# Kernel optimization log

Hardware: AMD Instinct MI355X
Metric: run time of the kernel (lower is better)

## Reference

```python
import jax, jax.numpy as jnp
import numpy as np

EMBED_DIM = 384
HEADS = 6
HEAD_DIM = EMBED_DIM // HEADS
WINDOW = 64


def setup_inputs() -> dict:
    key = jax.random.key(0)
    ks = jax.random.split(key, 5)
    B, T = 128, 256
    s_attn = 1.0 / np.sqrt(EMBED_DIM)
    x = jax.random.normal(ks[0], (B, T, EMBED_DIM), dtype=jnp.float32)
    W_attn = jax.random.normal(ks[1], (EMBED_DIM, 3 * EMBED_DIM), dtype=jnp.float32) * s_attn
    b_attn = jax.random.normal(ks[2], (3 * EMBED_DIM,), dtype=jnp.float32) * 0.02
    W_proj = jax.random.normal(ks[3], (EMBED_DIM, EMBED_DIM), dtype=jnp.float32) * s_attn
    b_proj = jax.random.normal(ks[4], (EMBED_DIM,), dtype=jnp.float32) * 0.02
    return {"x": x, "W_attn": W_attn, "b_attn": b_attn, "W_proj": W_proj, "b_proj": b_proj}


def reference(x, W_attn, b_attn, W_proj, b_proj):
    B, T, C = x.shape
    qkv = x @ W_attn + b_attn  # [B,T,3C]
    q, k, v = jnp.split(qkv, 3, axis=-1)
    # [B, H, T, hd]
    q = q.reshape(B, T, HEADS, HEAD_DIM).transpose(0, 2, 1, 3)
    k = k.reshape(B, T, HEADS, HEAD_DIM).transpose(0, 2, 1, 3)
    v = v.reshape(B, T, HEADS, HEAD_DIM).transpose(0, 2, 1, 3)
    scale = 1.0 / np.sqrt(HEAD_DIM).astype(np.float32)
    att = jnp.einsum('bhqd,bhkd->bhqk', q, k) * scale
    i = jnp.arange(T)
    causal = i[:, None] >= i[None, :]
    local = jnp.abs(i[:, None] - i[None, :]) <= WINDOW
    mask = (causal & local)[None, None, :, :]
    att = jnp.where(mask, att, -jnp.inf)
    att = jax.nn.softmax(att, axis=-1)
    y = jnp.einsum('bhqk,bhkd->bhqd', att, v)
    y = y.transpose(0, 2, 1, 3).reshape(B, T, C)
    return y @ W_proj + b_proj
```

## Files before the change

kernel.cpp:

```cpp
#include <hip/hip_runtime.h>

#define B_SZ   128
#define T_SEQ  256
#define C_DIM  384
#define HEADS  6
#define HD     64
#define WIN    64

typedef __bf16 bf16x8 __attribute__((ext_vector_type(8)));
typedef float  f32x4  __attribute__((ext_vector_type(4)));

typedef __attribute__((address_space(3))) void lds_void;
typedef __attribute__((address_space(1))) void gbl_void;

__device__ __forceinline__ unsigned short f2bf(float f) {
  unsigned u = __float_as_uint(f);
  u += 0x7FFFu + ((u >> 16) & 1u);
  return (unsigned short)(u >> 16);
}


__global__ __launch_bounds__(256) void convert_pack_f32_bf16(
    const float* __restrict__ in, unsigned short* __restrict__ out) {
  const int tid = blockIdx.x * 256 + threadIdx.x;
  const int m   = tid / 48;
  const int rem = tid % 48;
  const int kc  = rem >> 2;
  const int u   = rem & 3;
  const float4 a = *(const float4*)(in + (size_t)m * 384 + kc * 32 + u * 8);
  const float4 b = *(const float4*)(in + (size_t)m * 384 + kc * 32 + u * 8 + 4);
  const int p = u ^ ((m & 7) >> 1);
  unsigned short* dst =
      out + ((size_t)(m >> 7) * 12 + kc) * 4096 + (m & 127) * 32 + p * 8;
  ushort4 o1, o2;
  o1.x = f2bf(a.x); o1.y = f2bf(a.y); o1.z = f2bf(a.z); o1.w = f2bf(a.w);
  o2.x = f2bf(b.x); o2.y = f2bf(b.y); o2.z = f2bf(b.z); o2.w = f2bf(b.w);
  *(ushort4*)dst = o1;
  *(ushort4*)(dst + 4) = o2;
}

__global__ __launch_bounds__(256) void transpose_convert_pack(
    const float* __restrict__ in, unsigned short* __restrict__ out,
    int K, int N) {
  __shared__ float tile[32][33];
  const int gx = blockIdx.x * 32;
  const int gy = blockIdx.y * 32;
  const int tx = threadIdx.x;
  const int ty = threadIdx.y;
#pragma unroll
  for (int r = ty; r < 32; r += 8)
    tile[r][tx] = in[(size_t)(gy + r) * N + gx + tx];
  __syncthreads();
  const int nkc = K >> 5;
#pragma unroll
  for (int r = ty; r < 32; r += 8) {
    const int n = gx + r;
    const int k = gy + tx;
    const int p = (((k >> 3) & 3) ^ ((n & 7) >> 1));
    out[((size_t)(n >> 7) * nkc + (k >> 5)) * 4096 + (n & 127) * 32 + p * 8 +
        (k & 7)] = f2bf(tile[tx][r]);
  }
}

template <bool OUT_BF16, int KK>
__global__ __launch_bounds__(512, 4) void gemm_mfma_bf16(
    const unsigned short* __restrict__ A,
    const unsigned short* __restrict__ Bt,
    const float* __restrict__ bias,
    void* __restrict__ Cv, int M, int N, int tiles_n) {
  __shared__ __attribute__((aligned(16))) char smem_raw[73728];
  float* ep = (float*)smem_raw;

  constexpr int NK = KK / 32;

  const int t    = threadIdx.x;
  const int lane = t & 63;
  const int w    = t >> 6;
  const int wr   = w >> 1;
  const int wc   = w & 1;

  const unsigned id    = blockIdx.x;
  const unsigned remap = (id & 7u) * (gridDim.x >> 3) + (id >> 3);
  const int by = remap / (unsigned)tiles_n;
  const int bx = remap % (unsigned)tiles_n;
  const int m0 = by * 256;
  const int n0 = bx * 128;

  const unsigned short* Ap0 = A  + (size_t)(by * 2)     * NK * 4096;
  const unsigned short* Ap1 = A  + (size_t)(by * 2 + 1) * NK * 4096;
  const unsigned short* Btile = Bt + (size_t)bx * NK * 4096;

  const int m16  = lane & 15;
  const int quad = lane >> 4;
  const int cp   = (quad ^ ((m16 >> 1) & 3)) << 3;

  f32x4 acc[4][4];
#pragma unroll
  for (int i = 0; i < 4; ++i)
#pragma unroll
    for (int j = 0; j < 4; ++j) acc[i][j] = (f32x4){0.f, 0.f, 0.f, 0.f};

  auto stage = [&](int slot, int kc) {
    unsigned short* As = (unsigned short*)(smem_raw + slot * 24576);
    unsigned short* Bs = As + 256 * 32;
#pragma unroll
    for (int i = 0; i < 3; ++i) {
      const int idx = w * 3 + i;
      if (idx < 16) {
        const unsigned short* src =
            ((idx >> 3) ? Ap1 : Ap0) + (size_t)kc * 4096 + (idx & 7) * 512 +
            lane * 8;
        __builtin_amdgcn_global_load_lds((const gbl_void*)src,
                                         (lds_void*)(As + idx * 512), 16, 0, 0);
      } else {
        const int sub = idx - 16;
        const unsigned short* src =
            Btile + (size_t)kc * 4096 + sub * 512 + lane * 8;
        __builtin_amdgcn_global_load_lds((const gbl_void*)src,
                                         (lds_void*)(Bs + sub * 512), 16, 0, 0);
      }
    }
  };

  stage(0, 0);
  stage(1, 1);

#pragma unroll
  for (int kt = 0; kt < NK; ++kt) {
    if (kt + 1 < NK)
      asm volatile("s_waitcnt vmcnt(3) lgkmcnt(0)" ::: "memory");
    else
      asm volatile("s_waitcnt vmcnt(0) lgkmcnt(0)" ::: "memory");
    __builtin_amdgcn_s_barrier();
    __builtin_amdgcn_sched_barrier(0);

    if (kt + 2 < NK) stage((kt + 2) % 3, kt + 2);

    const unsigned short* As =
        (const unsigned short*)(smem_raw + (kt % 3) * 24576);
    const unsigned short* Bs = As + 256 * 32;

    bf16x8 af[4];
#pragma unroll
    for (int mt = 0; mt < 4; ++mt)
      af[mt] = *(const bf16x8*)(As + (size_t)(wr * 64 + mt * 16 + m16) * 32 + cp);
#pragma unroll
    for (int nt = 0; nt < 4; ++nt) {
      bf16x8 bfr = *(const bf16x8*)(Bs + (size_t)(wc * 64 + nt * 16 + m16) * 32 + cp);
#pragma unroll
      for (int mt = 0; mt < 4; ++mt)
        acc[mt][nt] = __builtin_amdgcn_mfma_f32_16x16x32_bf16(
            af[mt], bfr, acc[mt][nt], 0, 0, 0);
    }
  }
  __syncthreads();

  float bv[4];
#pragma unroll
  for (int nt = 0; nt < 4; ++nt) bv[nt] = bias[n0 + wc * 64 + nt * 16 + m16];

  const int which = bx / 3;
  const int hbase = (bx % 3) * 2;

#pragma unroll
  for (int p = 0; p < 4; ++p) {
    if (p) __syncthreads();
    if (wr == p) {
#pragma unroll
      for (int mt = 0; mt < 4; ++mt)
#pragma unroll
        for (int nt = 0; nt < 4; ++nt)
#pragma unroll
          for (int r = 0; r < 4; ++r)
            ep[(mt * 16 + quad * 4 + r) * 132 + wc * 64 + nt * 16 + m16] =
                acc[mt][nt][r] + bv[nt];
    }
    __syncthreads();
#pragma unroll
    for (int cc = 0; cc < 4; ++cc) {
      const int chunk = cc * 512 + t;
      const int row = chunk >> 5;
      const int c4  = chunk & 31;
      const int grow = m0 + p * 64 + row;
      if (OUT_BF16) {
        const int hh  = c4 >> 4;
        const int g16 = c4 & 15;
        const int s   = (which == 2) ? 0 : (row & 7);
        const int col = hh * 64 + ((((g16 >> 1) ^ s) << 3) | ((g16 & 1) << 2));
        f32x4 v = *(const f32x4*)(ep + row * 132 + col);
        ushort4 o;
        o.x = f2bf(v[0]); o.y = f2bf(v[1]); o.z = f2bf(v[2]); o.w = f2bf(v[3]);
        const int b_ = grow >> 8;
        const int tp = grow & 255;
        *(ushort4*)((unsigned short*)Cv +
                    ((size_t)((b_ * 3 + which) * HEADS + hbase + hh) * T_SEQ +
                     tp) * HD + g16 * 4) = o;
      } else {
        f32x4 v = *(const f32x4*)(ep + row * 132 + c4 * 4);
        const int gcol = n0 + c4 * 4;
        *(f32x4*)((float*)Cv + (size_t)grow * N + gcol) = v;
      }
    }
  }
}

#define PSTR 68
__global__ __launch_bounds__(256) void attn_mfma(
    const unsigned short* __restrict__ qkv, unsigned short* __restrict__ y) {
  __shared__ unsigned short Qs[64 * 64];
  __shared__ unsigned short Ks[64 * 64];
  __shared__ unsigned short Vt[64 * 64];
  __shared__ float Pw[4][16 * PSTR];

  const unsigned id  = blockIdx.x;
  const unsigned bid = (id & 7u) * (gridDim.x >> 3) + (id >> 3);
  const int qt  = bid & 3;
  const int h   = (bid >> 2) % HEADS;
  const int b   = bid / (4 * HEADS);
  const int t   = threadIdx.x;
  const int lane = t & 63;
  const int w    = t >> 6;
  const int quad = lane >> 4;
  const int m16  = lane & 15;
  const int sw   = m16 & 7;

  const unsigned short* Qpane =
      qkv + ((size_t)((b * 3 + 0) * HEADS + h) * T_SEQ) * HD;
  const unsigned short* Kpane =
      qkv + ((size_t)((b * 3 + 1) * HEADS + h) * T_SEQ) * HD;
  const unsigned short* Vpane =
      qkv + ((size_t)((b * 3 + 2) * HEADS + h) * T_SEQ) * HD;
  const int qg0 = qt * 64;

#pragma unroll
  for (int i = 0; i < 2; ++i) {
    const int inst = w * 2 + i;
    __builtin_amdgcn_global_load_lds(
        (const gbl_void*)(Qpane + (size_t)qg0 * HD + inst * 512 + lane * 8),
        (lds_void*)(Qs + inst * 512), 16, 0, 0);
  }

  float m_r[4], l_r[4];
  f32x4 yacc[4];
#pragma unroll
  for (int r = 0; r < 4; ++r) { m_r[r] = -1e30f; l_r[r] = 0.f; }
#pragma unroll
  for (int dt = 0; dt < 4; ++dt) yacc[dt] = (f32x4){0.f, 0.f, 0.f, 0.f};

  const int nchunks  = (qt == 0) ? 1 : 2;
  const int kb_first = (qt == 0) ? 0 : (qg0 - 64);
  const int qrow_base = qg0 + w * 16 + quad * 4;

  for (int ch = 0; ch < nchunks; ++ch) {
    const int kb = kb_first + ch * 64;

    __syncthreads();

#pragma unroll
    for (int i = 0; i < 2; ++i) {
      const int inst = w * 2 + i;
      __builtin_amdgcn_global_load_lds(
          (const gbl_void*)(Kpane + (size_t)kb * HD + inst * 512 + lane * 8),
          (lds_void*)(Ks + inst * 512), 16, 0, 0);
    }
    {
      const int vkey = t & 63;
      const int kc = vkey >> 3, ke = vkey & 7;
      const int vd0  = (t >> 6) * 16;
      const unsigned short* gv = Vpane + (size_t)(kb + vkey) * HD + vd0;
#pragma unroll
      for (int u = 0; u < 4; ++u) {
        ushort4 vv = *(const ushort4*)(gv + u * 4);
#pragma unroll
        for (int jj = 0; jj < 4; ++jj) {
          const int d = vd0 + u * 4 + jj;
          const unsigned short val =
              (jj == 0) ? vv.x : (jj == 1) ? vv.y : (jj == 2) ? vv.z : vv.w;
          Vt[d * 64 + ((kc ^ (d & 7)) << 3) + ke] = val;
        }
      }
    }
    __syncthreads();

    f32x4 sacc[4];
#pragma unroll
    for (int nt = 0; nt < 4; ++nt) sacc[nt] = (f32x4){0.f, 0.f, 0.f, 0.f};
#pragma unroll
    for (int ks = 0; ks < 64; ks += 32) {
      const int cp = (((ks >> 3) + quad) ^ sw) << 3;
      bf16x8 aq = *(const bf16x8*)(Qs + (size_t)(w * 16 + m16) * 64 + cp);
#pragma unroll
      for (int nt = 0; nt < 4; ++nt) {
        bf16x8 kf = *(const bf16x8*)(Ks + (size_t)(nt * 16 + m16) * 64 + cp);
        sacc[nt] = __builtin_amdgcn_mfma_f32_16x16x32_bf16(aq, kf, sacc[nt], 0, 0, 0);
      }
    }

    float mc[4] = {-1e30f, -1e30f, -1e30f, -1e30f};
#pragma unroll
    for (int nt = 0; nt < 4; ++nt) {
      const int kg = kb + nt * 16 + m16;
#pragma unroll
      for (int r = 0; r < 4; ++r) {
        const int qg = qrow_base + r;
        const bool valid = (kg <= qg) && (qg - kg <= WIN);
        const float sv = valid ? (sacc[nt][r] * 0.125f) : -1e30f;
        sacc[nt][r] = sv;
        mc[r] = fmaxf(mc[r], sv);
      }
    }
#pragma unroll
    for (int r = 0; r < 4; ++r) {
#pragma unroll
      for (int x = 1; x <= 8; x <<= 1) mc[r] = fmaxf(mc[r], __shfl_xor(mc[r], x));
    }

#pragma unroll
    for (int r = 0; r < 4; ++r) {
      const float mn    = fmaxf(m_r[r], mc[r]);
      const float alpha = __expf(m_r[r] - mn);
      m_r[r] = mn;
      l_r[r] *= alpha;
#pragma unroll
      for (int dt = 0; dt < 4; ++dt) yacc[dt][r] *= alpha;
      float ls = 0.f;
#pragma unroll
      for (int nt = 0; nt < 4; ++nt) {
        const float p = __expf(sacc[nt][r] - mn);
        sacc[nt][r] = p;
        ls += p;
      }
#pragma unroll
      for (int x = 1; x <= 8; x <<= 1) ls += __shfl_xor(ls, x);
      l_r[r] += ls;
    }

#pragma unroll
    for (int nt = 0; nt < 4; ++nt)
#pragma unroll
      for (int r = 0; r < 4; ++r)
        Pw[w][(quad * 4 + r) * PSTR + nt * 16 + m16] = sacc[nt][r];

#pragma unroll
    for (int ks = 0; ks < 64; ks += 32) {
      f32x4 pa = *(const f32x4*)(&Pw[w][m16 * PSTR + ks + quad * 8]);
      f32x4 pb = *(const f32x4*)(&Pw[w][m16 * PSTR + ks + quad * 8 + 4]);
      bf16x8 ap;
#pragma unroll
      for (int j = 0; j < 4; ++j) {
        ap[j]     = (__bf16)pa[j];
        ap[4 + j] = (__bf16)pb[j];
      }
      const int cp = (((ks >> 3) + quad) ^ sw) << 3;
#pragma unroll
      for (int dt = 0; dt < 4; ++dt) {
        bf16x8 vf = *(const bf16x8*)(Vt + (size_t)(dt * 16 + m16) * 64 + cp);
        yacc[dt] = __builtin_amdgcn_mfma_f32_16x16x32_bf16(ap, vf, yacc[dt], 0, 0, 0);
      }
    }
  }

  float* epy = &Pw[0][0];
  float inv[4];
#pragma unroll
  for (int r = 0; r < 4; ++r) inv[r] = 1.f / l_r[r];
#pragma unroll
  for (int dt = 0; dt < 4; ++dt)
#pragma unroll
    for (int r = 0; r < 4; ++r)
      epy[(w * 16 + quad * 4 + r) * PSTR + dt * 16 + m16] = yacc[dt][r] * inv[r];
  __syncthreads();
#pragma unroll
  for (int cc = 0; cc < 4; ++cc) {
    const int chunk = cc * 256 + t;
    const int row = chunk >> 4;
    const int c4  = chunk & 15;
    f32x4 v = *(const f32x4*)(epy + row * PSTR + c4 * 4);
    ushort4 o;
    o.x = f2bf(v[0]); o.y = f2bf(v[1]); o.z = f2bf(v[2]); o.w = f2bf(v[3]);
    const int m = b * T_SEQ + qg0 + row;
    const int c = h * HD + c4 * 4;
    const int kc = c >> 5;
    const int u  = (c >> 3) & 3;
    const int p  = u ^ ((m & 7) >> 1);
    *(ushort4*)(y + ((size_t)(m >> 7) * 12 + kc) * 4096 + (m & 127) * 32 +
                p * 8 + (c & 7)) = o;
  }
}

extern "C" void kernel_launch(void* const* d_in, const int* in_sizes, int n_in,
                              void* d_out, int out_size, void* d_ws, size_t ws_size,
                              hipStream_t stream) {
  const float* x      = (const float*)d_in[0];
  const float* W_attn = (const float*)d_in[1];
  const float* b_attn = (const float*)d_in[2];
  const float* W_proj = (const float*)d_in[3];
  const float* b_proj = (const float*)d_in[4];
  float* out = (float*)d_out;

  const int M = B_SZ * T_SEQ;

  unsigned short* qkv_b = (unsigned short*)d_ws;
  unsigned short* y_b   = qkv_b + (size_t)M * (3 * C_DIM);
  unsigned short* x_b   = y_b   + (size_t)M * C_DIM;
  unsigned short* Wa_t  = x_b   + (size_t)M * C_DIM;
  unsigned short* Wp_t  = Wa_t  + (size_t)(3 * C_DIM) * C_DIM;

  {
    convert_pack_f32_bf16<<<dim3(M * 48 / 256), 256, 0, stream>>>(x, x_b);
    transpose_convert_pack<<<dim3((3 * C_DIM) / 32, C_DIM / 32), dim3(32, 8), 0,
                             stream>>>(W_attn, Wa_t, C_DIM, 3 * C_DIM);
    transpose_convert_pack<<<dim3(C_DIM / 32, C_DIM / 32), dim3(32, 8), 0,
                             stream>>>(W_proj, Wp_t, C_DIM, C_DIM);
  }

  gemm_mfma_bf16<true, C_DIM><<<dim3(9 * (M / 256)), 512, 0, stream>>>(
      x_b, Wa_t, b_attn, qkv_b, M, 3 * C_DIM, 9);

  attn_mfma<<<dim3(B_SZ * HEADS * (T_SEQ / 64)), 256, 0, stream>>>(qkv_b, y_b);

  gemm_mfma_bf16<false, C_DIM><<<dim3(3 * (M / 256)), 512, 0, stream>>>(
      y_b, Wp_t, b_proj, out, M, C_DIM, 3);
}
```

Before: 189.3 us.

## Fuse fp32-to-bf16 conversion of x into the QKV GEMM A-tile loader

Removes the separate x conversion kernel and its bf16 staging buffer. The QKV GEMM now reads fp32 x straight into registers, converts it to bf16 and writes swizzled LDS tiles, while B still arrives through global_load_lds with a triple-buffered pipeline and manual waitcnt/barrier scheduling. This saves one launch plus a full write and re-read of x in bf16. In exchange the GEMM reads twice as many A bytes (fp32), each of the 9 column tiles converts the same rows again, and it needs more registers.

```diff
diff --git a/kernel.cpp b/kernel.cpp
--- a/kernel.cpp
+++ b/kernel.cpp
@@ -9,6 +9,7 @@
 
 typedef __bf16 bf16x8 __attribute__((ext_vector_type(8)));
 typedef float  f32x4  __attribute__((ext_vector_type(4)));
+typedef unsigned short u16x8 __attribute__((ext_vector_type(8)));
 
 typedef __attribute__((address_space(3))) void lds_void;
 typedef __attribute__((address_space(1))) void gbl_void;
@@ -19,25 +20,6 @@
   return (unsigned short)(u >> 16);
 }
 
-
-__global__ __launch_bounds__(256) void convert_pack_f32_bf16(
-    const float* __restrict__ in, unsigned short* __restrict__ out) {
-  const int tid = blockIdx.x * 256 + threadIdx.x;
-  const int m   = tid / 48;
-  const int rem = tid % 48;
-  const int kc  = rem >> 2;
-  const int u   = rem & 3;
-  const float4 a = *(const float4*)(in + (size_t)m * 384 + kc * 32 + u * 8);
-  const float4 b = *(const float4*)(in + (size_t)m * 384 + kc * 32 + u * 8 + 4);
-  const int p = u ^ ((m & 7) >> 1);
-  unsigned short* dst =
-      out + ((size_t)(m >> 7) * 12 + kc) * 4096 + (m & 127) * 32 + p * 8;
-  ushort4 o1, o2;
-  o1.x = f2bf(a.x); o1.y = f2bf(a.y); o1.z = f2bf(a.z); o1.w = f2bf(a.w);
-  o2.x = f2bf(b.x); o2.y = f2bf(b.y); o2.z = f2bf(b.z); o2.w = f2bf(b.w);
-  *(ushort4*)dst = o1;
-  *(ushort4*)(dst + 4) = o2;
-}
 
 __global__ __launch_bounds__(256) void transpose_convert_pack(
     const float* __restrict__ in, unsigned short* __restrict__ out,
@@ -62,12 +44,167 @@
   }
 }
 
-template <bool OUT_BF16, int KK>
+__global__ __launch_bounds__(512, 4) void gemm1_fused(
+    const float* __restrict__ X,
+    const unsigned short* __restrict__ Bt,
+    const float* __restrict__ bias,
+    unsigned short* __restrict__ qkv) {
+  __shared__ __attribute__((aligned(16))) char smem_raw[73728];
+  float* ep = (float*)smem_raw;
+
+  constexpr int NK = 12;
+
+  const int t    = threadIdx.x;
+  const int lane = t & 63;
+  const int w    = t >> 6;
+  const int wr   = w >> 1;
+  const int wc   = w & 1;
+
+  const unsigned id    = blockIdx.x;
+  const unsigned remap = (id & 7u) * (gridDim.x >> 3) + (id >> 3);
+  const int by = remap / 9u;
+  const int bx = remap % 9u;
+  const int m0 = by * 256;
+  const int n0 = bx * 128;
+
+  const unsigned short* Btile = Bt + (size_t)bx * NK * 4096;
+
+  const int m16  = lane & 15;
+  const int quad = lane >> 4;
+  const int cp   = (quad ^ ((m16 >> 1) & 3)) << 3;
+
+  const int arow  = t >> 1;
+  const int ahalf = t & 1;
+  const int sw_r  = (arow & 7) >> 1;
+  const int g0    = ahalf * 2;
+  const float* Arow = X + (size_t)(m0 + arow) * 384 + ahalf * 16;
+
+  f32x4 acc[4][4];
+#pragma unroll
+  for (int i = 0; i < 4; ++i)
+#pragma unroll
+    for (int j = 0; j < 4; ++j) acc[i][j] = (f32x4){0.f, 0.f, 0.f, 0.f};
+
+  f32x4 rA[2][4];
+
+  auto loadB = [&](int slot, int kc) {
+    unsigned short* Bs =
+        (unsigned short*)(smem_raw + slot * 24576) + 256 * 32;
+    const unsigned short* src = Btile + (size_t)kc * 4096 + w * 512 + lane * 8;
+    __builtin_amdgcn_global_load_lds((const gbl_void*)src,
+                                     (lds_void*)(Bs + w * 512), 16, 0, 0);
+  };
+  auto loadA = [&](int buf, int kc) {
+    const float* ap = Arow + kc * 32;
+#pragma unroll
+    for (int j = 0; j < 4; ++j) rA[buf][j] = *(const f32x4*)(ap + j * 4);
+  };
+  auto writeA = [&](int buf, int slot) {
+    unsigned short* As = (unsigned short*)(smem_raw + slot * 24576);
+    u16x8 v0, v1;
+#pragma unroll
+    for (int j = 0; j < 8; ++j) {
+      v0[j] = f2bf(rA[buf][j >> 2][j & 3]);
+      v1[j] = f2bf(rA[buf][2 + (j >> 2)][j & 3]);
+    }
+    *(u16x8*)(As + arow * 32 + ((g0 ^ sw_r) << 3))       = v0;
+    *(u16x8*)(As + arow * 32 + (((g0 + 1) ^ sw_r) << 3)) = v1;
+  };
+
+  loadB(0, 0); loadA(0, 0);
+  loadB(1, 1); loadA(1, 1);
+  asm volatile("s_waitcnt vmcnt(5)" ::: "memory");
+  writeA(0, 0);
+  asm volatile("s_waitcnt lgkmcnt(0)" ::: "memory");
+  __builtin_amdgcn_s_barrier();
+  __builtin_amdgcn_sched_barrier(0);
+
+#pragma unroll
+  for (int kt = 0; kt < NK; ++kt) {
+    if (kt + 2 < NK) {
+      loadB((kt + 2) % 3, kt + 2);
+      loadA(kt & 1, kt + 2);
+    }
+
+    const unsigned short* As =
+        (const unsigned short*)(smem_raw + (kt % 3) * 24576);
+    const unsigned short* Bs = As + 256 * 32;
+
+    bf16x8 af[4];
+#pragma unroll
+    for (int mt = 0; mt < 4; ++mt)
+      af[mt] = *(const bf16x8*)(As + (size_t)(wr * 64 + mt * 16 + m16) * 32 + cp);
+#pragma unroll
+    for (int nt = 0; nt < 4; ++nt) {
+      bf16x8 bfr = *(const bf16x8*)(Bs + (size_t)(wc * 64 + nt * 16 + m16) * 32 + cp);
+#pragma unroll
+      for (int mt = 0; mt < 4; ++mt)
+        acc[mt][nt] = __builtin_amdgcn_mfma_f32_16x16x32_bf16(
+            af[mt], bfr, acc[mt][nt], 0, 0, 0);
+    }
+
+    if (kt + 1 < NK) {
+      if (kt + 2 < NK)
+        asm volatile("s_waitcnt vmcnt(5)" ::: "memory");
+      else
+        asm volatile("s_waitcnt vmcnt(0)" ::: "memory");
+      writeA((kt + 1) & 1, (kt + 1) % 3);
+      asm volatile("s_waitcnt lgkmcnt(0)" ::: "memory");
+      __builtin_amdgcn_s_barrier();
+      __builtin_amdgcn_sched_barrier(0);
+    }
+  }
+  __syncthreads();
+
+  float bv[4];
+#pragma unroll
+  for (int nt = 0; nt < 4; ++nt) bv[nt] = bias[n0 + wc * 64 + nt * 16 + m16];
+
+  const int which = bx / 3;
+  const int hbase = (bx % 3) * 2;
+
+#pragma unroll
+  for (int p = 0; p < 4; ++p) {
+    if (p) __syncthreads();
+    if (wr == p) {
+#pragma unroll
+      for (int mt = 0; mt < 4; ++mt)
+#pragma unroll
+        for (int nt = 0; nt < 4; ++nt)
+#pragma unroll
+          for (int r = 0; r < 4; ++r)
+            ep[(mt * 16 + quad * 4 + r) * 132 + wc * 64 + nt * 16 + m16] =
+                acc[mt][nt][r] + bv[nt];
+    }
+    __syncthreads();
+#pragma unroll
+    for (int cc = 0; cc < 4; ++cc) {
+      const int chunk = cc * 512 + t;
+      const int row = chunk >> 5;
+      const int c4  = chunk & 31;
+      const int grow = m0 + p * 64 + row;
+      const int hh  = c4 >> 4;
+      const int g16 = c4 & 15;
+      const int s   = (which == 2) ? 0 : (row & 7);
+      const int col = hh * 64 + ((((g16 >> 1) ^ s) << 3) | ((g16 & 1) << 2));
+      f32x4 v = *(const f32x4*)(ep + row * 132 + col);
+      ushort4 o;
+      o.x = f2bf(v[0]); o.y = f2bf(v[1]); o.z = f2bf(v[2]); o.w = f2bf(v[3]);
+      const int b_ = grow >> 8;
+      const int tp = grow & 255;
+      *(ushort4*)(qkv +
+                  ((size_t)((b_ * 3 + which) * HEADS + hbase + hh) * T_SEQ +
+                   tp) * HD + g16 * 4) = o;
+    }
+  }
+}
+
+template <int KK>
 __global__ __launch_bounds__(512, 4) void gemm_mfma_bf16(
     const unsigned short* __restrict__ A,
     const unsigned short* __restrict__ Bt,
     const float* __restrict__ bias,
-    void* __restrict__ Cv, int M, int N, int tiles_n) {
+    float* __restrict__ Cv, int M, int N, int tiles_n) {
   __shared__ __attribute__((aligned(16))) char smem_raw[73728];
   float* ep = (float*)smem_raw;
 
@@ -159,9 +296,6 @@
 #pragma unroll
   for (int nt = 0; nt < 4; ++nt) bv[nt] = bias[n0 + wc * 64 + nt * 16 + m16];
 
-  const int which = bx / 3;
-  const int hbase = (bx % 3) * 2;
-
 #pragma unroll
   for (int p = 0; p < 4; ++p) {
     if (p) __syncthreads();
@@ -182,24 +316,8 @@
       const int row = chunk >> 5;
       const int c4  = chunk & 31;
       const int grow = m0 + p * 64 + row;
-      if (OUT_BF16) {
-        const int hh  = c4 >> 4;
-        const int g16 = c4 & 15;
-        const int s   = (which == 2) ? 0 : (row & 7);
-        const int col = hh * 64 + ((((g16 >> 1) ^ s) << 3) | ((g16 & 1) << 2));
-        f32x4 v = *(const f32x4*)(ep + row * 132 + col);
-        ushort4 o;
-        o.x = f2bf(v[0]); o.y = f2bf(v[1]); o.z = f2bf(v[2]); o.w = f2bf(v[3]);
-        const int b_ = grow >> 8;
-        const int tp = grow & 255;
-        *(ushort4*)((unsigned short*)Cv +
-                    ((size_t)((b_ * 3 + which) * HEADS + hbase + hh) * T_SEQ +
-                     tp) * HD + g16 * 4) = o;
-      } else {
-        f32x4 v = *(const f32x4*)(ep + row * 132 + c4 * 4);
-        const int gcol = n0 + c4 * 4;
-        *(f32x4*)((float*)Cv + (size_t)grow * N + gcol) = v;
-      }
+      f32x4 v = *(const f32x4*)(ep + row * 132 + c4 * 4);
+      *(f32x4*)(Cv + (size_t)grow * N + n0 + c4 * 4) = v;
     }
   }
 }
@@ -402,23 +520,18 @@
 
   unsigned short* qkv_b = (unsigned short*)d_ws;
   unsigned short* y_b   = qkv_b + (size_t)M * (3 * C_DIM);
-  unsigned short* x_b   = y_b   + (size_t)M * C_DIM;
-  unsigned short* Wa_t  = x_b   + (size_t)M * C_DIM;
+  unsigned short* Wa_t  = y_b   + (size_t)M * C_DIM;
   unsigned short* Wp_t  = Wa_t  + (size_t)(3 * C_DIM) * C_DIM;
 
-  {
-    convert_pack_f32_bf16<<<dim3(M * 48 / 256), 256, 0, stream>>>(x, x_b);
-    transpose_convert_pack<<<dim3((3 * C_DIM) / 32, C_DIM / 32), dim3(32, 8), 0,
-                             stream>>>(W_attn, Wa_t, C_DIM, 3 * C_DIM);
-    transpose_convert_pack<<<dim3(C_DIM / 32, C_DIM / 32), dim3(32, 8), 0,
-                             stream>>>(W_proj, Wp_t, C_DIM, C_DIM);
-  }
-
-  gemm_mfma_bf16<true, C_DIM><<<dim3(9 * (M / 256)), 512, 0, stream>>>(
-      x_b, Wa_t, b_attn, qkv_b, M, 3 * C_DIM, 9);
+  transpose_convert_pack<<<dim3((3 * C_DIM) / 32, C_DIM / 32), dim3(32, 8), 0,
+                           stream>>>(W_attn, Wa_t, C_DIM, 3 * C_DIM);
+  transpose_convert_pack<<<dim3(C_DIM / 32, C_DIM / 32), dim3(32, 8), 0,
+                           stream>>>(W_proj, Wp_t, C_DIM, C_DIM);
+
+  gemm1_fused<<<dim3(9 * (M / 256)), 512, 0, stream>>>(x, Wa_t, b_attn, qkv_b);
 
   attn_mfma<<<dim3(B_SZ * HEADS * (T_SEQ / 64)), 256, 0, stream>>>(qkv_b, y_b);
 
-  gemm_mfma_bf16<false, C_DIM><<<dim3(3 * (M / 256)), 512, 0, stream>>>(
+  gemm_mfma_bf16<C_DIM><<<dim3(3 * (M / 256)), 512, 0, stream>>>(
       y_b, Wp_t, b_proj, out, M, C_DIM, 3);
 }
```

Result: slower. 271.7 us (+43.5%).
